# Kernel tuning notes

Measured on AMD Instinct MI355X. Metric: run time of the kernel, lower is better.

Reference implementation:

```python
import jax, jax.numpy as jnp
import numpy as np

DIM, WIDTH = 5, 64
BATCH, N_SAVE = 4096, 64
RTOL, ATOL = 1e-3, 1e-6
SAFETY, FMIN, FMAX = 0.9, 0.2, 10.0
MAX_STEPS, DT0, EPS = 64, 0.1, 1e-6

# Tsit5 (Tsitouras 2011) Butcher tableau
A21 = 0.161
A31, A32 = -0.008480655492356989, 0.335480655492357
A41, A42, A43 = 2.8971530571054935, -6.359448489975075, 4.3622954328695815
A51, A52, A53, A54 = 5.325864828439257, -11.748883564062828, 7.4955393428898365, -0.09249506636175525
A61, A62, A63, A64, A65 = 5.86145544294642, -12.92096931784711, 8.159367898576159, -0.071584973281401, -0.028269050394068383
B1, B2, B3, B4, B5, B6 = 0.09646076681806523, 0.01, 0.4798896504144996, 1.379008574103742, -3.290069515436081, 2.324710524099774
# embedded 4th-order error coefficients (b - bhat)
E1, E2, E3, E4, E5, E6, E7 = (-0.00178001105222577714, -0.0008164344596567469,
    0.007880878010261995, -0.1447110071732629, 0.5823571654525552,
    -0.45808210592918697, 0.015151515151515152)


def _mlp(y, W1, b1, W2, b2, W3, b3, W4, b4):
    # eqx.nn.MLP(5, 5, width 64, depth 3, softplus)
    h = jax.nn.softplus(y @ W1.T + b1)
    h = jax.nn.softplus(h @ W2.T + b2)
    h = jax.nn.softplus(h @ W3.T + b3)
    return h @ W4.T + b4


def _solve_one(y0, t_eval, params):
    f = lambda y: _mlp(y, *params)
    t0, t1 = t_eval[0], t_eval[-1]
    # save points at/before t0 get y0
    ys0 = jnp.where((t_eval <= t0 + EPS)[:, None], y0[None, :], 0.0)

    def body(carry, _):
        t, y, h, ys = carry
        done = t >= t1 - EPS
        hc = jnp.where(done, 0.0, jnp.minimum(h, t1 - t))  # clip last step to t1
        k1 = f(y)
        k2 = f(y + hc * (A21 * k1))
        k3 = f(y + hc * (A31 * k1 + A32 * k2))
        k4 = f(y + hc * (A41 * k1 + A42 * k2 + A43 * k3))
        k5 = f(y + hc * (A51 * k1 + A52 * k2 + A53 * k3 + A54 * k4))
        k6 = f(y + hc * (A61 * k1 + A62 * k2 + A63 * k3 + A64 * k4 + A65 * k5))
        ynew = y + hc * (B1 * k1 + B2 * k2 + B3 * k3 + B4 * k4 + B5 * k5 + B6 * k6)
        k7 = f(ynew)  # FSAL stage, also used for error + interpolation
        err = hc * (E1 * k1 + E2 * k2 + E3 * k3 + E4 * k4 + E5 * k5 + E6 * k6 + E7 * k7)
        scale = ATOL + RTOL * jnp.maximum(jnp.abs(y), jnp.abs(ynew))
        enorm = jnp.sqrt(jnp.mean((err / scale) ** 2))
        enorm_c = jax.lax.stop_gradient(jnp.maximum(enorm, 1e-10))
        accept = enorm <= 1.0
        factor = jnp.clip(SAFETY * enorm_c ** -0.2, FMIN, FMAX)  # I-controller, order 5
        step_ok = accept & ~done
        t_next = jnp.where(step_ok, t + hc, t)
        y_next = jnp.where(step_ok, ynew, y)
        h_next = jnp.where(done, h, hc * factor)
        # cubic Hermite interpolation for save points inside (t, t_next]
        s = ((t_eval - t) / jnp.maximum(hc, 1e-12))[:, None]
        h00 = 2 * s**3 - 3 * s**2 + 1
        h10 = s**3 - 2 * s**2 + s
        h01 = -2 * s**3 + 3 * s**2
        h11 = s**3 - s**2
        yi = h00 * y + h10 * hc * k1 + h01 * ynew + h11 * hc * k7
        mask = (t_eval > t) & (t_eval <= t_next + EPS) & step_ok
        ys = jnp.where(mask[:, None], yi, ys)
        return (t_next, y_next, h_next, ys), None

    h0 = jnp.asarray(DT0, dtype=y0.dtype)
    (_, _, _, ys), _ = jax.lax.scan(body, (t0, y0, h0, ys0), None, length=MAX_STEPS)
    return ys  # [N_SAVE, DIM]


def setup_inputs() -> dict:
    key = jax.random.key(0)
    ks = jax.random.split(key, 9)
    y0 = jax.random.normal(ks[0], (BATCH, DIM), dtype=jnp.float32)
    t_eval = jnp.linspace(0.0, 1.0, N_SAVE, dtype=jnp.float32)

    def lin(k, out_d, in_d):
        lim = 1.0 / np.sqrt(in_d)
        kw, kb = jax.random.split(k)
        W = jax.random.uniform(kw, (out_d, in_d), jnp.float32, -lim, lim)
        b = jax.random.uniform(kb, (out_d,), jnp.float32, -lim, lim)
        return W, b

    W1, b1 = lin(ks[1], WIDTH, DIM)
    W2, b2 = lin(ks[2], WIDTH, WIDTH)
    W3, b3 = lin(ks[3], WIDTH, WIDTH)
    W4, b4 = lin(ks[4], DIM, WIDTH)
    return {"y0": y0, "t_eval": t_eval, "W1": W1, "b1": b1, "W2": W2, "b2": b2,
            "W3": W3, "b3": b3, "W4": W4, "b4": b4}


def reference(y0, t_eval, W1, b1, W2, b2, W3, b3, W4, b4):
    params = (W1, b1, W2, b2, W3, b3, W4, b4)
    return jax.vmap(lambda y: _solve_one(y, t_eval, params))(y0)  # [BATCH, N_SAVE, DIM]
```

## Files before the change

kernel.cpp:

```cpp
#include <hip/hip_runtime.h>
#include <cmath>

namespace {

constexpr int kDim = 5;
constexpr int kSave = 64;
constexpr int kTraj = 16;
constexpr int kThreads = 256;
constexpr int kMaxSteps = 64;
constexpr int ZS = 40;
constexpr int HS = 72;
constexpr int SD = 8;

typedef _Float16 half8 __attribute__((ext_vector_type(8)));
typedef float f32x4 __attribute__((ext_vector_type(4)));

__device__ __forceinline__ float softplusf(float x) {
  return fmaxf(x, 0.0f) + __logf(1.0f + __expf(-fabsf(x)));
}

__device__ __forceinline__ void lds_fence() {
  asm volatile("s_waitcnt lgkmcnt(0)" ::: "memory");
}

__global__ __launch_bounds__(kThreads, 1)
void node_tsit5_kernel(const float* __restrict__ gy0,
                       const float* __restrict__ gte,
                       const float* __restrict__ gW1, const float* __restrict__ gb1,
                       const float* __restrict__ gW2, const float* __restrict__ gb2,
                       const float* __restrict__ gW3, const float* __restrict__ gb3,
                       const float* __restrict__ gW4, const float* __restrict__ gb4,
                       float* __restrict__ out) {
  const float A21 = 0.161f;
  const float A31 = -0.008480655492356989f, A32 = 0.335480655492357f;
  const float A41 = 2.8971530571054935f, A42 = -6.359448489975075f, A43 = 4.3622954328695815f;
  const float A51 = 5.325864828439257f, A52 = -11.748883564062828f, A53 = 7.4955393428898365f,
              A54 = -0.09249506636175525f;
  const float A61 = 5.86145544294642f, A62 = -12.92096931784711f, A63 = 8.159367898576159f,
              A64 = -0.071584973281401f, A65 = -0.028269050394068383f;
  const float B1 = 0.09646076681806523f, B2 = 0.01f, B3 = 0.4798896504144996f,
              B4 = 1.379008574103742f, B5 = -3.290069515436081f, B6 = 2.324710524099774f;
  const float E1 = -0.00178001105222577714f, E2 = -0.0008164344596567469f,
              E3 = 0.007880878010261995f, E4 = -0.1447110071732629f, E5 = 0.5823571654525552f,
              E6 = -0.45808210592918697f, E7 = 0.015151515151515152f;

  __shared__ __align__(16) _Float16 zbp[4][kTraj * ZS];
  __shared__ __align__(16) _Float16 h0[kTraj * HS], l0[kTraj * HS];
  __shared__ __align__(16) _Float16 h1[kTraj * HS], l1[kTraj * HS];
  __shared__ __align__(16) _Float16 h2[kTraj * HS], l2[kTraj * HS];
  __shared__ __align__(16) float ySs[4][kTraj * SD], ynS[4][kTraj * SD];
  __shared__ __align__(16) float k1S[4][kTraj * SD], k7S[4][kTraj * SD];
  __shared__ float ctT[4][kTraj], ctH[4][kTraj], ctN[4][kTraj], ctO[4][kTraj];

  const int tid = threadIdx.x;
  const int bid = blockIdx.x;
  const int w = tid >> 6;
  const int ln = tid & 63;
  const int quad = ln >> 4;
  const int col = ln & 15;
  const int row0 = quad * 4;
  const int nn = (w << 4) | col;
  const bool cact = col < kDim;

  half8 w1c, w2h[2], w3h[2], w4h[2];
  #pragma unroll
  for (int j = 0; j < 8; ++j) {
    int kk2 = quad * 8 + j;
    float wv = 0.0f;
    if (kk2 < 5) wv = gW1[nn * 5 + kk2];
    else if (kk2 < 10) wv = gW1[nn * 5 + (kk2 - 5)];
    w1c[j] = (_Float16)wv;
  }
  #pragma unroll
  for (int kf = 0; kf < 2; ++kf)
    #pragma unroll
    for (int j = 0; j < 8; ++j) {
      int kk2 = kf * 32 + quad * 8 + j;
      w2h[kf][j] = (_Float16)gW2[nn * 64 + kk2];
      w3h[kf][j] = (_Float16)gW3[nn * 64 + kk2];
      w4h[kf][j] = cact ? (_Float16)gW4[col * 64 + kk2] : (_Float16)0.0f;
    }
  const float c1 = gb1[nn], c2 = gb2[nn], c3 = gb3[nn];
  const float c4 = cact ? gb4[col] : 0.0f;

  const float t0v = gte[0];
  const float t1v = gte[kSave - 1];
  float teq[4];
  #pragma unroll
  for (int q = 0; q < 4; ++q) teq[q] = gte[16 * w + 4 * quad + q];

  for (int i = ln; i < kTraj * ZS; i += 64) zbp[w][i] = (_Float16)0.0f;

  f32x4 syr = {0, 0, 0, 0}, synr = {0, 0, 0, 0}, kk[7];
  if (cact) {
    #pragma unroll
    for (int r = 0; r < 4; ++r) {
      float v = gy0[(size_t)(bid * kTraj + row0 + r) * kDim + col];
      syr[r] = v;
      _Float16 hi = (_Float16)v;
      zbp[w][(row0 + r) * ZS + col] = hi;
      zbp[w][(row0 + r) * ZS + col + 5] = (_Float16)(v - (float)hi);
      ySs[w][(row0 + r) * SD + col] = v;
    }
  }
  lds_fence();

  {
    int tt = ln & 15;
    float y0v[kDim];
    #pragma unroll
    for (int d = 0; d < kDim; ++d) y0v[d] = ySs[w][tt * SD + d];
    #pragma unroll
    for (int q = 0; q < 4; ++q) {
      int n = 16 * w + 4 * quad + q;
      bool isy0 = teq[q] <= t0v + 1e-6f;
      float* op = out + ((size_t)(bid * kTraj + tt) * kSave + n) * kDim;
      #pragma unroll
      for (int d = 0; d < kDim; ++d) op[d] = isy0 ? y0v[d] : 0.0f;
    }
  }

  auto evalF = [&]() -> f32x4 {
    {
      half8 az = *(const half8*)(zbp[w] + col * ZS + quad * 8);
      f32x4 a = {c1, c1, c1, c1};
      a = __builtin_amdgcn_mfma_f32_16x16x32_f16(az, w1c, a, 0, 0, 0);
      #pragma unroll
      for (int r = 0; r < 4; ++r) {
        float s = softplusf(a[r]);
        _Float16 hi = (_Float16)s;
        h0[(row0 + r) * HS + nn] = hi;
        l0[(row0 + r) * HS + nn] = (_Float16)(s - (float)hi);
      }
    }
    __syncthreads();
    {
      half8 ah0 = *(const half8*)(h0 + col * HS + quad * 8);
      half8 ah1 = *(const half8*)(h0 + col * HS + 32 + quad * 8);
      half8 al0 = *(const half8*)(l0 + col * HS + quad * 8);
      half8 al1 = *(const half8*)(l0 + col * HS + 32 + quad * 8);
      f32x4 a = {c2, c2, c2, c2};
      f32x4 b = {0, 0, 0, 0};
      a = __builtin_amdgcn_mfma_f32_16x16x32_f16(ah0, w2h[0], a, 0, 0, 0);
      b = __builtin_amdgcn_mfma_f32_16x16x32_f16(al0, w2h[0], b, 0, 0, 0);
      a = __builtin_amdgcn_mfma_f32_16x16x32_f16(ah1, w2h[1], a, 0, 0, 0);
      b = __builtin_amdgcn_mfma_f32_16x16x32_f16(al1, w2h[1], b, 0, 0, 0);
      a += b;
      #pragma unroll
      for (int r = 0; r < 4; ++r) {
        float s = softplusf(a[r]);
        _Float16 hi = (_Float16)s;
        h1[(row0 + r) * HS + nn] = hi;
        l1[(row0 + r) * HS + nn] = (_Float16)(s - (float)hi);
      }
    }
    __syncthreads();
    {
      half8 ah0 = *(const half8*)(h1 + col * HS + quad * 8);
      half8 ah1 = *(const half8*)(h1 + col * HS + 32 + quad * 8);
      half8 al0 = *(const half8*)(l1 + col * HS + quad * 8);
      half8 al1 = *(const half8*)(l1 + col * HS + 32 + quad * 8);
      f32x4 a = {c3, c3, c3, c3};
      f32x4 b = {0, 0, 0, 0};
      a = __builtin_amdgcn_mfma_f32_16x16x32_f16(ah0, w3h[0], a, 0, 0, 0);
      b = __builtin_amdgcn_mfma_f32_16x16x32_f16(al0, w3h[0], b, 0, 0, 0);
      a = __builtin_amdgcn_mfma_f32_16x16x32_f16(ah1, w3h[1], a, 0, 0, 0);
      b = __builtin_amdgcn_mfma_f32_16x16x32_f16(al1, w3h[1], b, 0, 0, 0);
      a += b;
      #pragma unroll
      for (int r = 0; r < 4; ++r) {
        float s = softplusf(a[r]);
        _Float16 hi = (_Float16)s;
        h2[(row0 + r) * HS + nn] = hi;
        l2[(row0 + r) * HS + nn] = (_Float16)(s - (float)hi);
      }
    }
    __syncthreads();
    f32x4 a = {c4, c4, c4, c4};
    {
      half8 ah0 = *(const half8*)(h2 + col * HS + quad * 8);
      half8 ah1 = *(const half8*)(h2 + col * HS + 32 + quad * 8);
      half8 al0 = *(const half8*)(l2 + col * HS + quad * 8);
      half8 al1 = *(const half8*)(l2 + col * HS + 32 + quad * 8);
      f32x4 b = {0, 0, 0, 0};
      a = __builtin_amdgcn_mfma_f32_16x16x32_f16(ah0, w4h[0], a, 0, 0, 0);
      b = __builtin_amdgcn_mfma_f32_16x16x32_f16(al0, w4h[0], b, 0, 0, 0);
      a = __builtin_amdgcn_mfma_f32_16x16x32_f16(ah1, w4h[1], a, 0, 0, 0);
      b = __builtin_amdgcn_mfma_f32_16x16x32_f16(al1, w4h[1], b, 0, 0, 0);
      a += b;
    }
    return a;
  };

  auto zwrite = [&](f32x4 z) {
    if (cact) {
      #pragma unroll
      for (int r = 0; r < 4; ++r) {
        _Float16 hi = (_Float16)z[r];
        zbp[w][(row0 + r) * ZS + col] = hi;
        zbp[w][(row0 + r) * ZS + col + 5] = (_Float16)(z[r] - (float)hi);
      }
    }
    lds_fence();
  };

  kk[0] = evalF();

  f32x4 tcur = {t0v, t0v, t0v, t0v};
  f32x4 hcur = {0.1f, 0.1f, 0.1f, 0.1f};

  for (int step = 0; step < kMaxSteps; ++step) {
    f32x4 hcs, tOldr;
    bool dnr[4];
    bool all4 = true;
    #pragma unroll
    for (int r = 0; r < 4; ++r) {
      bool d = tcur[r] >= t1v - 1e-6f;
      dnr[r] = d;
      all4 &= d;
      hcs[r] = d ? 0.0f : fminf(hcur[r], t1v - tcur[r]);
      tOldr[r] = tcur[r];
    }
    if (__ballot(all4) == ~0ull) break;

    f32x4 z;
    #pragma unroll
    for (int r = 0; r < 4; ++r) z[r] = fmaf(hcs[r], A21 * kk[0][r], syr[r]);
    zwrite(z); kk[1] = evalF();

    #pragma unroll
    for (int r = 0; r < 4; ++r)
      z[r] = fmaf(hcs[r], fmaf(A32, kk[1][r], A31 * kk[0][r]), syr[r]);
    zwrite(z); kk[2] = evalF();

    #pragma unroll
    for (int r = 0; r < 4; ++r)
      z[r] = fmaf(hcs[r], fmaf(A43, kk[2][r], fmaf(A42, kk[1][r], A41 * kk[0][r])), syr[r]);
    zwrite(z); kk[3] = evalF();

    #pragma unroll
    for (int r = 0; r < 4; ++r)
      z[r] = fmaf(hcs[r], fmaf(A54, kk[3][r], fmaf(A53, kk[2][r],
                  fmaf(A52, kk[1][r], A51 * kk[0][r]))), syr[r]);
    zwrite(z); kk[4] = evalF();

    #pragma unroll
    for (int r = 0; r < 4; ++r)
      z[r] = fmaf(hcs[r], fmaf(A65, kk[4][r], fmaf(A64, kk[3][r], fmaf(A63, kk[2][r],
                  fmaf(A62, kk[1][r], A61 * kk[0][r])))), syr[r]);
    zwrite(z); kk[5] = evalF();

    #pragma unroll
    for (int r = 0; r < 4; ++r)
      synr[r] = fmaf(hcs[r], fmaf(B6, kk[5][r], fmaf(B5, kk[4][r], fmaf(B4, kk[3][r],
                 fmaf(B3, kk[2][r], fmaf(B2, kk[1][r], B1 * kk[0][r]))))), syr[r]);
    zwrite(synr); kk[6] = evalF();

    f32x4 rr2;
    #pragma unroll
    for (int r = 0; r < 4; ++r) {
      float err = hcs[r] * fmaf(E7, kk[6][r], fmaf(E6, kk[5][r], fmaf(E5, kk[4][r],
                  fmaf(E4, kk[3][r], fmaf(E3, kk[2][r], fmaf(E2, kk[1][r], E1 * kk[0][r]))))));
      float sc = fmaf(1e-3f, fmaxf(fabsf(syr[r]), fabsf(synr[r])), 1e-6f);
      float rr = err / sc;
      rr2[r] = cact ? rr * rr : 0.0f;
    }
    #pragma unroll
    for (int m = 1; m < 16; m <<= 1) {
      #pragma unroll
      for (int r = 0; r < 4; ++r) rr2[r] += __shfl_xor(rr2[r], m, 64);
    }

    bool okr[4];
    #pragma unroll
    for (int r = 0; r < 4; ++r) {
      float enorm = __fsqrt_rn(rr2[r] * 0.2f);
      float enc = fmaxf(enorm, 1e-10f);
      bool accept = enorm <= 1.0f;
      float factor = fminf(fmaxf(0.9f * __expf(-0.2f * __logf(enc)), 0.2f), 10.0f);
      bool ok = accept && !dnr[r];
      okr[r] = ok;
      tcur[r] = ok ? tcur[r] + hcs[r] : tcur[r];
      hcur[r] = dnr[r] ? hcur[r] : hcs[r] * factor;
    }

    if (cact) {
      #pragma unroll
      for (int r = 0; r < 4; ++r) {
        int o = (row0 + r) * SD + col;
        ySs[w][o] = syr[r];
        ynS[w][o] = synr[r];
        k1S[w][o] = kk[0][r];
        k7S[w][o] = kk[6][r];
      }
    }
    if (col == 0) {
      #pragma unroll
      for (int r = 0; r < 4; ++r) {
        int m = row0 + r;
        ctT[w][m] = tOldr[r];
        ctH[w][m] = hcs[r];
        ctN[w][m] = tcur[r];
        ctO[w][m] = okr[r] ? 1.0f : 0.0f;
      }
    }
    lds_fence();

    {
      int tt = ln & 15;
      if (ctO[w][tt] != 0.0f) {
        float tOld = ctT[w][tt], hcv = ctH[w][tt], tNew = ctN[w][tt];
        float inv = 1.0f / fmaxf(hcv, 1e-12f);
        const float* yb = &ySs[w][tt * SD];
        const float* nb = &ynS[w][tt * SD];
        const float* ab = &k1S[w][tt * SD];
        const float* bb = &k7S[w][tt * SD];
        float yv[kDim], ynv[kDim], k1v[kDim], k7v[kDim];
        #pragma unroll
        for (int d = 0; d < kDim; ++d) {
          yv[d] = yb[d];
          ynv[d] = nb[d];
          k1v[d] = hcv * ab[d];
          k7v[d] = hcv * bb[d];
        }
        #pragma unroll
        for (int q = 0; q < 4; ++q) {
          float te = teq[q];
          if (te > tOld && te <= tNew + 1e-6f) {
            int n = 16 * w + 4 * quad + q;
            float sx = (te - tOld) * inv;
            float s2 = sx * sx, s3 = s2 * sx;
            float h00 = 2.f * s3 - 3.f * s2 + 1.f;
            float h10 = s3 - 2.f * s2 + sx;
            float h01 = -2.f * s3 + 3.f * s2;
            float h11 = s3 - s2;
            float* op = out + ((size_t)(bid * kTraj + tt) * kSave + n) * kDim;
            #pragma unroll
            for (int d = 0; d < kDim; ++d)
              op[d] = h00 * yv[d] + h10 * k1v[d] + h01 * ynv[d] + h11 * k7v[d];
          }
        }
      }
    }

    #pragma unroll
    for (int r = 0; r < 4; ++r) {
      if (okr[r]) { syr[r] = synr[r]; kk[0][r] = kk[6][r]; }
    }
  }
}

}

extern "C" void kernel_launch(void* const* d_in, const int* in_sizes, int n_in,
                              void* d_out, int out_size, void* d_ws, size_t ws_size,
                              hipStream_t stream) {
  const float* y0 = (const float*)d_in[0];
  const float* te = (const float*)d_in[1];
  const float* W1 = (const float*)d_in[2];
  const float* b1 = (const float*)d_in[3];
  const float* W2 = (const float*)d_in[4];
  const float* b2 = (const float*)d_in[5];
  const float* W3 = (const float*)d_in[6];
  const float* b3 = (const float*)d_in[7];
  const float* W4 = (const float*)d_in[8];
  const float* b4 = (const float*)d_in[9];
  float* out = (float*)d_out;

  const int batch = in_sizes[0] / kDim;
  const int blocks = batch / kTraj;
  hipLaunchKernelGGL(node_tsit5_kernel, dim3(blocks), dim3(kThreads), 0, stream,
                     y0, te, W1, b1, W2, b2, W3, b3, W4, b4, out);
}
```

Measured before the change: 110.6 us.

## Share single z buffer across waves with block barriers and exact error norm

```diff
diff --git a/kernel.cpp b/kernel.cpp
--- a/kernel.cpp
+++ b/kernel.cpp
@@ -44,7 +44,7 @@
               E3 = 0.007880878010261995f, E4 = -0.1447110071732629f, E5 = 0.5823571654525552f,
               E6 = -0.45808210592918697f, E7 = 0.015151515151515152f;
 
-  __shared__ __align__(16) _Float16 zbp[4][kTraj * ZS];
+  __shared__ __align__(16) _Float16 zb[kTraj * ZS];
   __shared__ __align__(16) _Float16 h0[kTraj * HS], l0[kTraj * HS];
   __shared__ __align__(16) _Float16 h1[kTraj * HS], l1[kTraj * HS];
   __shared__ __align__(16) _Float16 h2[kTraj * HS], l2[kTraj * HS];
@@ -61,6 +61,7 @@
   const int row0 = quad * 4;
   const int nn = (w << 4) | col;
   const bool cact = col < kDim;
+  const bool w0 = (w == 0);
 
   half8 w1c, w2h[2], w3h[2], w4h[2];
   #pragma unroll
@@ -89,7 +90,8 @@
   #pragma unroll
   for (int q = 0; q < 4; ++q) teq[q] = gte[16 * w + 4 * quad + q];
 
-  for (int i = ln; i < kTraj * ZS; i += 64) zbp[w][i] = (_Float16)0.0f;
+  for (int i = tid; i < kTraj * ZS; i += kThreads) zb[i] = (_Float16)0.0f;
+  __syncthreads();
 
   f32x4 syr = {0, 0, 0, 0}, synr = {0, 0, 0, 0}, kk[7];
   if (cact) {
@@ -97,13 +99,15 @@
     for (int r = 0; r < 4; ++r) {
       float v = gy0[(size_t)(bid * kTraj + row0 + r) * kDim + col];
       syr[r] = v;
-      _Float16 hi = (_Float16)v;
-      zbp[w][(row0 + r) * ZS + col] = hi;
-      zbp[w][(row0 + r) * ZS + col + 5] = (_Float16)(v - (float)hi);
       ySs[w][(row0 + r) * SD + col] = v;
+      if (w0) {
+        _Float16 hi = (_Float16)v;
+        zb[(row0 + r) * ZS + col] = hi;
+        zb[(row0 + r) * ZS + col + 5] = (_Float16)(v - (float)hi);
+      }
     }
   }
-  lds_fence();
+  __syncthreads();
 
   {
     int tt = ln & 15;
@@ -122,7 +126,7 @@
 
   auto evalF = [&]() -> f32x4 {
     {
-      half8 az = *(const half8*)(zbp[w] + col * ZS + quad * 8);
+      half8 az = *(const half8*)(zb + col * ZS + quad * 8);
       f32x4 a = {c1, c1, c1, c1};
       a = __builtin_amdgcn_mfma_f32_16x16x32_f16(az, w1c, a, 0, 0, 0);
       #pragma unroll
@@ -193,15 +197,15 @@
   };
 
   auto zwrite = [&](f32x4 z) {
-    if (cact) {
+    if (w0 && cact) {
       #pragma unroll
       for (int r = 0; r < 4; ++r) {
         _Float16 hi = (_Float16)z[r];
-        zbp[w][(row0 + r) * ZS + col] = hi;
-        zbp[w][(row0 + r) * ZS + col + 5] = (_Float16)(z[r] - (float)hi);
-      }
-    }
-    lds_fence();
+        zb[(row0 + r) * ZS + col] = hi;
+        zb[(row0 + r) * ZS + col + 5] = (_Float16)(z[r] - (float)hi);
+      }
+    }
+    __syncthreads();
   };
 
   kk[0] = evalF();
@@ -265,19 +269,17 @@
       float rr = err / sc;
       rr2[r] = cact ? rr * rr : 0.0f;
     }
-    #pragma unroll
-    for (int m = 1; m < 16; m <<= 1) {
-      #pragma unroll
-      for (int r = 0; r < 4; ++r) rr2[r] += __shfl_xor(rr2[r], m, 64);
-    }
-
     bool okr[4];
     #pragma unroll
     for (int r = 0; r < 4; ++r) {
-      float enorm = __fsqrt_rn(rr2[r] * 0.2f);
+      float s = 0.0f;
+      #pragma unroll
+      for (int d = 0; d < kDim; ++d)
+        s += __shfl(rr2[r], quad * 16 + d, 64);
+      float enorm = sqrtf(s / 5.0f);
       float enc = fmaxf(enorm, 1e-10f);
       bool accept = enorm <= 1.0f;
-      float factor = fminf(fmaxf(0.9f * __expf(-0.2f * __logf(enc)), 0.2f), 10.0f);
+      float factor = fminf(fmaxf(0.9f * powf(enc, -0.2f), 0.2f), 10.0f);
       bool ok = accept && !dnr[r];
       okr[r] = ok;
       tcur[r] = ok ? tcur[r] + hcs[r] : tcur[r];
```

New measurement: 113.8 us. 2.9% more time.
